# Kernel tuning notes

Hardware: AMD Instinct MI355X
Metric: run time of the kernel (lower is better)

The kernel has to match this reference:

```python
import jax, jax.numpy as jnp
import numpy as np

N = 50000      # num nodes
E = 1_600_000  # num edges
D = 64         # in_dim == hidden_dim
H = 4          # heads
C = 16         # head_dim = hidden_dim // heads
NEG = 0.2      # leaky_relu negative slope (PyG GATConv default)


def setup_inputs() -> dict:
    key = jax.random.key(0)
    ks = jax.random.split(key, 20)
    f = lambda k, s: (jax.random.normal(k, s, jnp.float32) * 0.1)
    return dict(
        node_features=jax.random.normal(ks[0], (N, D), jnp.float32),
        edge_index=jax.random.randint(ks[1], (2, E), 0, N, dtype=jnp.int32),
        edge_type=jax.random.randint(ks[2], (E,), 0, 5, dtype=jnp.int32),
        edge_attr=jax.random.normal(ks[3], (E, 1), jnp.float32),
        # GAT layer 1 (PyG GATConv: lin has no bias, att_* are [H,C], final bias [H*C])
        W1=f(ks[4], (D, H * C)), att_src1=f(ks[5], (H, C)), att_dst1=f(ks[6], (H, C)),
        We1=f(ks[7], (1, H * C)), att_e1=f(ks[8], (H, C)), b1=jnp.zeros((H * C,), jnp.float32),
        # GAT layer 2
        W2=f(ks[9], (D, H * C)), att_src2=f(ks[10], (H, C)), att_dst2=f(ks[11], (H, C)),
        We2=f(ks[12], (1, H * C)), att_e2=f(ks[13], (H, C)), b2=jnp.zeros((H * C,), jnp.float32),
        # LayerNorms
        g1=jnp.ones((D,), jnp.float32), beta1=jnp.zeros((D,), jnp.float32),
        g2=jnp.ones((D,), jnp.float32), beta2=jnp.zeros((D,), jnp.float32),
        # output head
        Wout=f(ks[14], (D, 1)), bout=jnp.zeros((1,), jnp.float32),
    )


def _layernorm(x, g, b, eps=1e-5):
    mu = x.mean(-1, keepdims=True)
    v = ((x - mu) ** 2).mean(-1, keepdims=True)
    return (x - mu) * jax.lax.rsqrt(v + eps) * g + b


def _seg_softmax(alpha, dst, n):
    # numerically stable segment softmax over incoming edges of each dst node
    m = jax.ops.segment_max(alpha, dst, num_segments=n)
    m = jnp.where(jnp.isfinite(m), m, 0.0)
    ex = jnp.exp(alpha - m[dst])
    den = jax.ops.segment_sum(ex, dst, num_segments=n)
    return ex / (den[dst] + 1e-16)


def _gatconv(x, src, dst, eattr, W, a_s, a_d, We, a_e, b, n):
    xs = (x @ W).reshape(n, H, C)                       # [N,H,C]
    a_src = jnp.einsum('nhc,hc->nh', xs, a_s)           # [N,H]
    a_dst = jnp.einsum('nhc,hc->nh', xs, a_d)           # [N,H]
    ee = (eattr @ We).reshape(-1, H, C)                 # [E',H,C]
    a_edge = jnp.einsum('ehc,hc->eh', ee, a_e)          # [E',H]
    alpha = a_src[src] + a_dst[dst] + a_edge            # [E',H]
    alpha = jax.nn.leaky_relu(alpha, NEG)
    alpha = _seg_softmax(alpha, dst, n)                 # [E',H]
    msg = xs[src] * alpha[..., None]                    # [E',H,C] gather-weighted messages
    out = jax.ops.segment_sum(msg, dst, num_segments=n) # scatter-aggregate
    return out.reshape(n, H * C) + b


def reference(node_features, edge_index, edge_type, edge_attr,
              W1, att_src1, att_dst1, We1, att_e1, b1,
              W2, att_src2, att_dst2, We2, att_e2, b2,
              g1, beta1, g2, beta2, Wout, bout):
    src, dst = edge_index[0], edge_index[1]
    # PyG add_self_loops(fill_value='mean'): self-loop edge_attr = mean of edge_attr over incoming edges
    cnt = jax.ops.segment_sum(jnp.ones((E,), jnp.float32), dst, num_segments=N)
    loop_attr = jax.ops.segment_sum(edge_attr, dst, num_segments=N) / jnp.maximum(cnt, 1.0)[:, None]
    loops = jnp.arange(N, dtype=src.dtype)
    src2 = jnp.concatenate([src, loops])
    dst2 = jnp.concatenate([dst, loops])
    ea = jnp.concatenate([edge_attr, loop_attr], axis=0)

    residual = node_features  # in_dim == hidden_dim -> no res_proj
    h = _gatconv(node_features, src2, dst2, ea, W1, att_src1, att_dst1, We1, att_e1, b1, N)
    h = jax.nn.elu(_layernorm(h + residual, g1, beta1))
    residual = h
    h = _gatconv(h, src2, dst2, ea, W2, att_src2, att_dst2, We2, att_e2, b2, N)
    h = jax.nn.elu(_layernorm(h + residual, g2, beta2))
    return h @ Wout + bout
```

## Files before the change

### kernel.cpp

```cpp
#include <hip/hip_runtime.h>
#include <hip/hip_bf16.h>
#include <cfloat>

#define NN 50000
#define NE 1600000
#define NEG 0.2f
#define NBKT 1563
#define BNODE 32
#define P1_TILE 2048
#define P1_BLOCKS 782
#define BCAP 1280
#define SLOTS 96
#define L2E 1.4426950408889634f

typedef __attribute__((ext_vector_type(8))) short bf8_t;
typedef __attribute__((ext_vector_type(4))) float f4_t;

__device__ __forceinline__ float bf16bits_to_f(unsigned v) {
  return __uint_as_float(v << 16);
}
__device__ __forceinline__ unsigned f_to_bf16bits(float f) {
  unsigned u = __float_as_uint(f);
  return (u + 0x7fffu + ((u >> 16) & 1u)) >> 16;
}

__global__ __launch_bounds__(256) void prep_kernel(
    const float* __restrict__ W1, const float* __restrict__ as1,
    const float* __restrict__ ad1, unsigned short* __restrict__ We1,
    const float* __restrict__ W2, const float* __restrict__ as2,
    const float* __restrict__ ad2, unsigned short* __restrict__ We2) {
  const float* W = blockIdx.x ? W2 : W1;
  const float* as = blockIdx.x ? as2 : as1;
  const float* ad = blockIdx.x ? ad2 : ad1;
  unsigned short* Wx = blockIdx.x ? We2 : We1;
  int t = threadIdx.x;
  if (t < 64) {
    const float* wr = W + t * 64;
#pragma unroll
    for (int h = 0; h < 4; ++h) {
      float ps = 0.f, pd = 0.f;
#pragma unroll
      for (int c = 0; c < 16; ++c) {
        ps = fmaf(wr[h * 16 + c], as[h * 16 + c], ps);
        pd = fmaf(wr[h * 16 + c], ad[h * 16 + c], pd);
      }
      Wx[t * 80 + 64 + h] = (unsigned short)f_to_bf16bits(ps * L2E);
      Wx[t * 80 + 68 + h] = (unsigned short)f_to_bf16bits(pd * L2E);
    }
#pragma unroll
    for (int j = 72; j < 80; ++j) Wx[t * 80 + j] = 0;
  }
  for (int i = t; i < 4096; i += 256) {
    int k = i >> 6, n = i & 63;
    Wx[k * 80 + n] = (unsigned short)f_to_bf16bits(W[i]);
  }
}

__global__ __launch_bounds__(256) void bin_kernel(
    const int* __restrict__ src, const int* __restrict__ dst,
    const float* __restrict__ ea, int* __restrict__ gcnt,
    int2* __restrict__ gbuf) {
  __shared__ int lcnt[NBKT];
  __shared__ int lcur[NBKT];
  int t = threadIdx.x;
  for (int i = t; i < NBKT; i += 256) lcnt[i] = 0;
  __syncthreads();
  int e0 = blockIdx.x * P1_TILE;
  int bb[8], vx[8], vy[8];
#pragma unroll
  for (int k = 0; k < 8; ++k) {
    int e = e0 + k * 256 + t;
    if (e < NE) {
      int d = dst[e];
      bb[k] = d >> 5;
      vx[k] = ((d & 31) << 16) | src[e];
      vy[k] = __float_as_int(ea[e]);
      atomicAdd(&lcnt[bb[k]], 1);
    } else {
      bb[k] = -1;
    }
  }
  __syncthreads();
  for (int i = t; i < NBKT; i += 256) lcur[i] = atomicAdd(&gcnt[i], lcnt[i]);
  __syncthreads();
#pragma unroll
  for (int k = 0; k < 8; ++k) {
    if (bb[k] >= 0) {
      int pos = atomicAdd(&lcur[bb[k]], 1);
      if (pos < BCAP) gbuf[(size_t)bb[k] * BCAP + pos] = make_int2(vx[k], vy[k]);
    }
  }
}

__global__ __launch_bounds__(256) void build_kernel(
    const int* __restrict__ gcnt, const int2* __restrict__ gbuf,
    int* __restrict__ cnt, unsigned* __restrict__ csr) {
  __shared__ int lc[BNODE];
  int t = threadIdx.x;
  int b = blockIdx.x;
  if (t < BNODE) lc[t] = 0;
  __syncthreads();
  int len = gcnt[b]; if (len > BCAP) len = BCAP;
  const int2* buf = gbuf + (size_t)b * BCAP;
  for (int i = t; i < len; i += 256) {
    int2 v = buf[i];
    int dl = (v.x >> 16) & 31;
    int s = v.x & 0xffff;
    int pos = atomicAdd(&lc[dl], 1);
    if (pos < SLOTS) {
      unsigned eb = ((unsigned)v.y) & 0xffff0000u;
      csr[(size_t)(b * BNODE + dl) * SLOTS + pos] = eb | (unsigned)s;
    }
  }
  __syncthreads();
  if (t < BNODE) {
    int n = b * BNODE + t;
    if (n < NN) cnt[n] = min(lc[t], SLOTS);
  }
}

__device__ __forceinline__ bf8_t pack8(const float* p) {
  bf8_t r;
#pragma unroll
  for (int i = 0; i < 8; ++i) r[i] = (short)f_to_bf16bits(p[i]);
  return r;
}

template <bool FP32IN>
__global__ __launch_bounds__(256) void gemm_mfma_kernel(
    const void* __restrict__ xin, const unsigned short* __restrict__ Wext,
    unsigned short* __restrict__ xsb, float* __restrict__ a_src,
    float* __restrict__ a_dst) {
  __shared__ unsigned short Wt[80][68];
  int t = threadIdx.x;
  for (int i = t; i < 5120; i += 256) {
    int k = i / 80, n = i - k * 80;
    Wt[n][k] = Wext[i];
  }
  __syncthreads();
  int lane = t & 63, wave = t >> 6;
  int quad = lane >> 4, n16 = lane & 15;

  bf8_t bfrag[5][2];
#pragma unroll
  for (int nt = 0; nt < 5; ++nt)
#pragma unroll
    for (int kk = 0; kk < 2; ++kk)
      bfrag[nt][kk] = *(const bf8_t*)&Wt[nt * 16 + n16][kk * 32 + quad * 8];

  int r0 = blockIdx.x * 64 + wave * 16;
  int rowA = r0 + n16; if (rowA > NN - 1) rowA = NN - 1;
  bf8_t af0, af1;
  if (FP32IN) {
    const float* xr = (const float*)xin + (size_t)rowA * 64 + quad * 8;
    af0 = pack8(xr);
    af1 = pack8(xr + 32);
  } else {
    const bf8_t* xrow =
        (const bf8_t*)((const unsigned short*)xin + (size_t)rowA * 64);
    af0 = xrow[quad];
    af1 = xrow[4 + quad];
  }
#pragma unroll
  for (int nt = 0; nt < 5; ++nt) {
    f4_t acc = {0.f, 0.f, 0.f, 0.f};
    acc = __builtin_amdgcn_mfma_f32_16x16x32_bf16(af0, bfrag[nt][0], acc, 0, 0, 0);
    acc = __builtin_amdgcn_mfma_f32_16x16x32_bf16(af1, bfrag[nt][1], acc, 0, 0, 0);
    if (nt < 4) {
#pragma unroll
      for (int reg = 0; reg < 4; ++reg) {
        int row = r0 + quad * 4 + reg;
        if (row < NN)
          xsb[(size_t)row * 64 + nt * 16 + n16] =
              (unsigned short)f_to_bf16bits(acc[reg]);
      }
    } else {
#pragma unroll
      for (int reg = 0; reg < 4; ++reg) {
        int row = r0 + quad * 4 + reg;
        if (row < NN && n16 < 8) {
          if (n16 < 4) a_src[row * 4 + n16] = acc[reg];
          else a_dst[row * 4 + (n16 - 4)] = acc[reg];
        }
      }
    }
  }
}

template <bool HEAD>
__global__ __launch_bounds__(256) void aggregate_kernel(
    const int* __restrict__ cnt, const unsigned* __restrict__ csr,
    const unsigned short* __restrict__ xsb, const float* __restrict__ a_src,
    const float* __restrict__ a_dst, const float* __restrict__ We,
    const float* __restrict__ att_e, const float* __restrict__ bias,
    const float* __restrict__ res, const float* __restrict__ g,
    const float* __restrict__ beta, const float* __restrict__ Wout,
    const float* __restrict__ bout, float* __restrict__ out,
    unsigned short* __restrict__ out_b) {
  __shared__ __align__(16) uint2 rec[4][64][4];
  int t = threadIdx.x;
  int lane = t & 63, wave = t >> 6;
  int n = blockIdx.x * 4 + wave;
  int d2 = lane & 31;
  int hb = d2 >> 3;
  int half = lane >> 5;

  float sp = We[lane] * att_e[lane];
#pragma unroll
  for (int off = 8; off; off >>= 1) sp += __shfl_xor(sp, off, 16);
  sp *= L2E;
  float s0 = __shfl(sp, 0, 64), s1 = __shfl(sp, 16, 64);
  float s2 = __shfl(sp, 32, 64), s3 = __shfl(sp, 48, 64);

  const float4 adv = *(const float4*)(a_dst + (size_t)n * 4);

  int dn = cnt[n];
  int r0 = n * SLOTS, r1 = r0 + dn;
  float accx = 0.f, accy = 0.f, den = 0.f, easum = 0.f;
  const uint2* rpb = &rec[wave][half][hb];
  const char* xd = (const char*)xsb + d2 * 4;

  for (int base = r0; base < r1; base += 64) {
    int c = r1 - base; if (c > 64) c = 64;
    int e = base + lane;
    unsigned ce = (e < r1) ? csr[e] : 0u;
    float ea = __uint_as_float(ce & 0xffff0000u);
    easum += ea;
    unsigned soff = (ce & 0xffffu) * 128u;
    float ex0 = 0.f, ex1 = 0.f, ex2 = 0.f, ex3 = 0.f;
    if (e < r1) {
      const float4 av = *(const float4*)(a_src + (size_t)(ce & 0xffffu) * 4);
      float a0 = av.x + fmaf(ea, s0, adv.x); a0 = fmaxf(a0, NEG * a0);
      float a1 = av.y + fmaf(ea, s1, adv.y); a1 = fmaxf(a1, NEG * a1);
      float a2 = av.z + fmaf(ea, s2, adv.z); a2 = fmaxf(a2, NEG * a2);
      float a3 = av.w + fmaf(ea, s3, adv.w); a3 = fmaxf(a3, NEG * a3);
      ex0 = exp2f(a0); ex1 = exp2f(a1); ex2 = exp2f(a2); ex3 = exp2f(a3);
    }
    uint4* wp = (uint4*)&rec[wave][lane][0];
    wp[0] = make_uint4(soff, __float_as_uint(ex0), soff, __float_as_uint(ex1));
    wp[1] = make_uint4(soff, __float_as_uint(ex2), soff, __float_as_uint(ex3));
    int c8 = (c + 7) & ~7;
    for (int j = 0; j < c8; j += 8) {
      uint2 va = rpb[j * 4];
      uint2 vb = rpb[j * 4 + 8];
      uint2 vc = rpb[j * 4 + 16];
      uint2 vd = rpb[j * 4 + 24];
      unsigned ua = *(const unsigned*)(xd + va.x);
      unsigned ub = *(const unsigned*)(xd + vb.x);
      unsigned uc = *(const unsigned*)(xd + vc.x);
      unsigned ud = *(const unsigned*)(xd + vd.x);
      float efa = __uint_as_float(va.y), efb = __uint_as_float(vb.y);
      float efc = __uint_as_float(vc.y), efd = __uint_as_float(vd.y);
      den += (efa + efb) + (efc + efd);
      accx = fmaf(efa, __uint_as_float(ua << 16), accx);
      accy = fmaf(efa, __uint_as_float(ua & 0xffff0000u), accy);
      accx = fmaf(efb, __uint_as_float(ub << 16), accx);
      accy = fmaf(efb, __uint_as_float(ub & 0xffff0000u), accy);
      accx = fmaf(efc, __uint_as_float(uc << 16), accx);
      accy = fmaf(efc, __uint_as_float(uc & 0xffff0000u), accy);
      accx = fmaf(efd, __uint_as_float(ud << 16), accx);
      accy = fmaf(efd, __uint_as_float(ud & 0xffff0000u), accy);
    }
  }

  den += __shfl_xor(den, 32, 64);
  accx += __shfl_xor(accx, 32, 64);
  accy += __shfl_xor(accy, 32, 64);
#pragma unroll
  for (int off = 32; off; off >>= 1) easum += __shfl_xor(easum, off, 64);

  float loop_ea = easum / fmaxf((float)dn, 1.0f);
  float as_h = a_src[(size_t)n * 4 + hb];
  float adn = (hb == 0) ? adv.x : (hb == 1) ? adv.y : (hb == 2) ? adv.z : adv.w;
  float sph = (hb == 0) ? s0 : (hb == 1) ? s1 : (hb == 2) ? s2 : s3;
  float a_self = as_h + fmaf(loop_ea, sph, adn);
  a_self = fmaxf(a_self, NEG * a_self);
  float ex_self = exp2f(a_self);
  den += ex_self;
  unsigned un = *(const unsigned*)((const char*)xsb + (size_t)n * 128 + d2 * 4);
  accx = fmaf(ex_self, __uint_as_float(un << 16), accx);
  accy = fmaf(ex_self, __uint_as_float(un & 0xffff0000u), accy);

  float rden = 1.f / (den + 1e-16f);
  const float2 bi = *(const float2*)(bias + d2 * 2);
  const float2 rsd = *(const float2*)(res + (size_t)n * 64 + d2 * 2);
  float vx = accx * rden + bi.x + rsd.x;
  float vy = accy * rden + bi.y + rsd.y;
  float s = vx + vy;
#pragma unroll
  for (int off = 32; off; off >>= 1) s += __shfl_xor(s, off, 64);
  float mu = s * (1.0f / 128.0f);
  float dx = vx - mu, dy = vy - mu;
  float var = dx * dx + dy * dy;
#pragma unroll
  for (int off = 32; off; off >>= 1) var += __shfl_xor(var, off, 64);
  var *= (1.0f / 128.0f);
  float rstd = rsqrtf(var + 1e-5f);
  const float2 gg = *(const float2*)(g + d2 * 2);
  const float2 bb = *(const float2*)(beta + d2 * 2);
  float yx = dx * rstd * gg.x + bb.x;
  float yy = dy * rstd * gg.y + bb.y;
  yx = yx > 0.f ? yx : expm1f(yx);
  yy = yy > 0.f ? yy : expm1f(yy);
  if (HEAD) {
    const float2 wv = *(const float2*)(Wout + d2 * 2);
    float p = yx * wv.x + yy * wv.y;
#pragma unroll
    for (int off = 32; off; off >>= 1) p += __shfl_xor(p, off, 64);
    if (lane == 0) out[n] = p * 0.5f + bout[0];
  } else if (lane < 32) {
    *(float2*)(out + (size_t)n * 64 + d2 * 2) = make_float2(yx, yy);
    unsigned ob = f_to_bf16bits(yx) | (f_to_bf16bits(yy) << 16);
    *(unsigned*)(out_b + (size_t)n * 64 + d2 * 2) = ob;
  }
}

extern "C" void kernel_launch(void* const* d_in, const int* in_sizes, int n_in,
                              void* d_out, int out_size, void* d_ws,
                              size_t ws_size, hipStream_t stream) {
  const float* node_features = (const float*)d_in[0];
  const int* edge_index = (const int*)d_in[1];
  const int* src = edge_index;
  const int* dst = edge_index + NE;
  const float* edge_attr = (const float*)d_in[3];
  const float* W1 = (const float*)d_in[4];
  const float* att_src1 = (const float*)d_in[5];
  const float* att_dst1 = (const float*)d_in[6];
  const float* We1 = (const float*)d_in[7];
  const float* att_e1 = (const float*)d_in[8];
  const float* b1 = (const float*)d_in[9];
  const float* W2 = (const float*)d_in[10];
  const float* att_src2 = (const float*)d_in[11];
  const float* att_dst2 = (const float*)d_in[12];
  const float* We2 = (const float*)d_in[13];
  const float* att_e2 = (const float*)d_in[14];
  const float* b2 = (const float*)d_in[15];
  const float* g1 = (const float*)d_in[16];
  const float* beta1 = (const float*)d_in[17];
  const float* g2 = (const float*)d_in[18];
  const float* beta2 = (const float*)d_in[19];
  const float* Wout = (const float*)d_in[20];
  const float* bout = (const float*)d_in[21];
  float* out = (float*)d_out;

  char* ws = (char*)d_ws;
  size_t o = 0;
  auto alloc = [&](size_t bytes) {
    void* p = ws + o;
    o += (bytes + 255) & ~(size_t)255;
    return p;
  };
  int* gcnt = (int*)alloc((size_t)NBKT * 4);
  int2* gbuf = (int2*)alloc((size_t)NBKT * BCAP * 8);
  int* cnt = (int*)alloc((size_t)NN * 4);
  unsigned* csr = (unsigned*)alloc((size_t)NN * SLOTS * 4);
  unsigned short* xsb = (unsigned short*)alloc((size_t)NN * 64 * 2);
  unsigned short* h1b = (unsigned short*)alloc((size_t)NN * 64 * 2);
  unsigned short* Wext1 = (unsigned short*)alloc(64 * 80 * 2);
  unsigned short* Wext2 = (unsigned short*)alloc(64 * 80 * 2);
  float* a_srcb = (float*)alloc((size_t)NN * 4 * 4);
  float* a_dstb = (float*)alloc((size_t)NN * 4 * 4);
  float* h1 = (float*)alloc((size_t)NN * 64 * 4);

  hipMemsetAsync(gcnt, 0, (size_t)NBKT * 4, stream);

  prep_kernel<<<2, 256, 0, stream>>>(W1, att_src1, att_dst1, Wext1, W2,
                                     att_src2, att_dst2, Wext2);

  bin_kernel<<<P1_BLOCKS, 256, 0, stream>>>(src, dst, edge_attr, gcnt, gbuf);
  build_kernel<<<NBKT, 256, 0, stream>>>(gcnt, gbuf, cnt, csr);

  gemm_mfma_kernel<true><<<782, 256, 0, stream>>>(node_features, Wext1, xsb,
                                                  a_srcb, a_dstb);
  aggregate_kernel<false><<<NN / 4, 256, 0, stream>>>(
      cnt, csr, xsb, a_srcb, a_dstb, We1, att_e1, b1, node_features, g1, beta1,
      nullptr, nullptr, h1, h1b);

  gemm_mfma_kernel<false><<<782, 256, 0, stream>>>(h1b, Wext2, xsb, a_srcb,
                                                   a_dstb);
  aggregate_kernel<true><<<NN / 4, 256, 0, stream>>>(
      cnt, csr, xsb, a_srcb, a_dstb, We2, att_e2, b2, h1, g2, beta2, Wout, bout,
      out, nullptr);
}
```

Measured before the change: 266.6 us.

## Fuse prep into GEMM, merge binning with first GEMM, drop fp32 h1

Removes the separate weight-prep kernel: each GEMM block now converts W to bf16 and computes the attention projection columns in shared memory. The edge-binning and first-layer GEMM run as one horizontally fused launch with disjoint block ranges. The layer-1 output is no longer written in fp32, and layer 2 reads its residual from the bf16 copy. This saves two launches and one large write/read, but each GEMM block repeats the weight preprocessing, and the residual loses precision by being stored in bf16.

New measurement: 255.4 us. 4.2% less time.

```diff
diff --git a/kernel.cpp b/kernel.cpp
--- a/kernel.cpp
+++ b/kernel.cpp
@@ -9,9 +9,11 @@
 #define BNODE 32
 #define P1_TILE 2048
 #define P1_BLOCKS 782
+#define GEMM_BLOCKS 782
 #define BCAP 1280
 #define SLOTS 96
 #define L2E 1.4426950408889634f
+#define SMEM_BYTES 12512
 
 typedef __attribute__((ext_vector_type(8))) short bf8_t;
 typedef __attribute__((ext_vector_type(4))) float f4_t;
@@ -24,48 +26,23 @@
   return (u + 0x7fffu + ((u >> 16) & 1u)) >> 16;
 }
 
-__global__ __launch_bounds__(256) void prep_kernel(
-    const float* __restrict__ W1, const float* __restrict__ as1,
-    const float* __restrict__ ad1, unsigned short* __restrict__ We1,
-    const float* __restrict__ W2, const float* __restrict__ as2,
-    const float* __restrict__ ad2, unsigned short* __restrict__ We2) {
-  const float* W = blockIdx.x ? W2 : W1;
-  const float* as = blockIdx.x ? as2 : as1;
-  const float* ad = blockIdx.x ? ad2 : ad1;
-  unsigned short* Wx = blockIdx.x ? We2 : We1;
-  int t = threadIdx.x;
-  if (t < 64) {
-    const float* wr = W + t * 64;
-#pragma unroll
-    for (int h = 0; h < 4; ++h) {
-      float ps = 0.f, pd = 0.f;
-#pragma unroll
-      for (int c = 0; c < 16; ++c) {
-        ps = fmaf(wr[h * 16 + c], as[h * 16 + c], ps);
-        pd = fmaf(wr[h * 16 + c], ad[h * 16 + c], pd);
-      }
-      Wx[t * 80 + 64 + h] = (unsigned short)f_to_bf16bits(ps * L2E);
-      Wx[t * 80 + 68 + h] = (unsigned short)f_to_bf16bits(pd * L2E);
-    }
-#pragma unroll
-    for (int j = 72; j < 80; ++j) Wx[t * 80 + j] = 0;
-  }
-  for (int i = t; i < 4096; i += 256) {
-    int k = i >> 6, n = i & 63;
-    Wx[k * 80 + n] = (unsigned short)f_to_bf16bits(W[i]);
-  }
-}
-
-__global__ __launch_bounds__(256) void bin_kernel(
-    const int* __restrict__ src, const int* __restrict__ dst,
-    const float* __restrict__ ea, int* __restrict__ gcnt,
-    int2* __restrict__ gbuf) {
-  __shared__ int lcnt[NBKT];
-  __shared__ int lcur[NBKT];
+__device__ __forceinline__ bf8_t pack8(const float* p) {
+  bf8_t r;
+#pragma unroll
+  for (int i = 0; i < 8; ++i) r[i] = (short)f_to_bf16bits(p[i]);
+  return r;
+}
+
+__device__ void bin_body(char* smem, int blk, const int* __restrict__ src,
+                         const int* __restrict__ dst,
+                         const float* __restrict__ ea, int* __restrict__ gcnt,
+                         int2* __restrict__ gbuf) {
+  int* lcnt = (int*)smem;
+  int* lcur = lcnt + NBKT;
   int t = threadIdx.x;
   for (int i = t; i < NBKT; i += 256) lcnt[i] = 0;
   __syncthreads();
-  int e0 = blockIdx.x * P1_TILE;
+  int e0 = blk * P1_TILE;
   int bb[8], vx[8], vy[8];
 #pragma unroll
   for (int k = 0; k < 8; ++k) {
@@ -92,50 +69,34 @@
   }
 }
 
-__global__ __launch_bounds__(256) void build_kernel(
-    const int* __restrict__ gcnt, const int2* __restrict__ gbuf,
-    int* __restrict__ cnt, unsigned* __restrict__ csr) {
-  __shared__ int lc[BNODE];
+template <bool FP32IN>
+__device__ void gemm_body(char* smem, int blk, const void* __restrict__ xin,
+                          const float* __restrict__ W,
+                          const float* __restrict__ att_s,
+                          const float* __restrict__ att_d,
+                          unsigned short* __restrict__ xsb,
+                          float* __restrict__ a_src,
+                          float* __restrict__ a_dst) {
+  unsigned short(*Wt)[68] = (unsigned short(*)[68])smem;
   int t = threadIdx.x;
-  int b = blockIdx.x;
-  if (t < BNODE) lc[t] = 0;
-  __syncthreads();
-  int len = gcnt[b]; if (len > BCAP) len = BCAP;
-  const int2* buf = gbuf + (size_t)b * BCAP;
-  for (int i = t; i < len; i += 256) {
-    int2 v = buf[i];
-    int dl = (v.x >> 16) & 31;
-    int s = v.x & 0xffff;
-    int pos = atomicAdd(&lc[dl], 1);
-    if (pos < SLOTS) {
-      unsigned eb = ((unsigned)v.y) & 0xffff0000u;
-      csr[(size_t)(b * BNODE + dl) * SLOTS + pos] = eb | (unsigned)s;
-    }
-  }
-  __syncthreads();
-  if (t < BNODE) {
-    int n = b * BNODE + t;
-    if (n < NN) cnt[n] = min(lc[t], SLOTS);
-  }
-}
-
-__device__ __forceinline__ bf8_t pack8(const float* p) {
-  bf8_t r;
-#pragma unroll
-  for (int i = 0; i < 8; ++i) r[i] = (short)f_to_bf16bits(p[i]);
-  return r;
-}
-
-template <bool FP32IN>
-__global__ __launch_bounds__(256) void gemm_mfma_kernel(
-    const void* __restrict__ xin, const unsigned short* __restrict__ Wext,
-    unsigned short* __restrict__ xsb, float* __restrict__ a_src,
-    float* __restrict__ a_dst) {
-  __shared__ unsigned short Wt[80][68];
-  int t = threadIdx.x;
-  for (int i = t; i < 5120; i += 256) {
-    int k = i / 80, n = i - k * 80;
-    Wt[n][k] = Wext[i];
+  for (int i = t; i < 4096; i += 256) {
+    int k = i >> 6, n = i & 63;
+    Wt[n][k] = (unsigned short)f_to_bf16bits(W[i]);
+  }
+  __syncthreads();
+  {
+    int k = t & 63, h = t >> 6;
+    float ps = 0.f, pd = 0.f;
+#pragma unroll
+    for (int c = 0; c < 16; ++c) {
+      float w = bf16bits_to_f(Wt[h * 16 + c][k]);
+      ps = fmaf(w, att_s[h * 16 + c], ps);
+      pd = fmaf(w, att_d[h * 16 + c], pd);
+    }
+    Wt[64 + h][k] = (unsigned short)f_to_bf16bits(ps * L2E);
+    Wt[68 + h][k] = (unsigned short)f_to_bf16bits(pd * L2E);
+    Wt[72 + h][k] = 0;
+    Wt[76 + h][k] = 0;
   }
   __syncthreads();
   int lane = t & 63, wave = t >> 6;
@@ -148,7 +109,7 @@
     for (int kk = 0; kk < 2; ++kk)
       bfrag[nt][kk] = *(const bf8_t*)&Wt[nt * 16 + n16][kk * 32 + quad * 8];
 
-  int r0 = blockIdx.x * 64 + wave * 16;
+  int r0 = blk * 64 + wave * 16;
   int rowA = r0 + n16; if (rowA > NN - 1) rowA = NN - 1;
   bf8_t af0, af1;
   if (FP32IN) {
@@ -187,13 +148,65 @@
   }
 }
 
+__global__ __launch_bounds__(256) void front_kernel(
+    const int* __restrict__ src, const int* __restrict__ dst,
+    const float* __restrict__ ea, int* __restrict__ gcnt,
+    int2* __restrict__ gbuf, const float* __restrict__ x,
+    const float* __restrict__ W1, const float* __restrict__ as1,
+    const float* __restrict__ ad1, unsigned short* __restrict__ xsb,
+    float* __restrict__ a_src, float* __restrict__ a_dst) {
+  __shared__ __align__(16) char smem[SMEM_BYTES];
+  if (blockIdx.x < P1_BLOCKS) {
+    bin_body(smem, blockIdx.x, src, dst, ea, gcnt, gbuf);
+  } else {
+    gemm_body<true>(smem, blockIdx.x - P1_BLOCKS, x, W1, as1, ad1, xsb, a_src,
+                    a_dst);
+  }
+}
+
+__global__ __launch_bounds__(256) void gemm2_kernel(
+    const unsigned short* __restrict__ xin, const float* __restrict__ W,
+    const float* __restrict__ att_s, const float* __restrict__ att_d,
+    unsigned short* __restrict__ xsb, float* __restrict__ a_src,
+    float* __restrict__ a_dst) {
+  __shared__ __align__(16) char smem[SMEM_BYTES];
+  gemm_body<false>(smem, blockIdx.x, xin, W, att_s, att_d, xsb, a_src, a_dst);
+}
+
+__global__ __launch_bounds__(256) void build_kernel(
+    const int* __restrict__ gcnt, const int2* __restrict__ gbuf,
+    int* __restrict__ cnt, unsigned* __restrict__ csr) {
+  __shared__ int lc[BNODE];
+  int t = threadIdx.x;
+  int b = blockIdx.x;
+  if (t < BNODE) lc[t] = 0;
+  __syncthreads();
+  int len = gcnt[b]; if (len > BCAP) len = BCAP;
+  const int2* buf = gbuf + (size_t)b * BCAP;
+  for (int i = t; i < len; i += 256) {
+    int2 v = buf[i];
+    int dl = (v.x >> 16) & 31;
+    int s = v.x & 0xffff;
+    int pos = atomicAdd(&lc[dl], 1);
+    if (pos < SLOTS) {
+      unsigned eb = ((unsigned)v.y) & 0xffff0000u;
+      csr[(size_t)(b * BNODE + dl) * SLOTS + pos] = eb | (unsigned)s;
+    }
+  }
+  __syncthreads();
+  if (t < BNODE) {
+    int n = b * BNODE + t;
+    if (n < NN) cnt[n] = min(lc[t], SLOTS);
+  }
+}
+
 template <bool HEAD>
 __global__ __launch_bounds__(256) void aggregate_kernel(
     const int* __restrict__ cnt, const unsigned* __restrict__ csr,
     const unsigned short* __restrict__ xsb, const float* __restrict__ a_src,
     const float* __restrict__ a_dst, const float* __restrict__ We,
     const float* __restrict__ att_e, const float* __restrict__ bias,
-    const float* __restrict__ res, const float* __restrict__ g,
+    const void* __restrict__ resv, const float* __restrict__ g,
     const float* __restrict__ beta, const float* __restrict__ Wout,
     const float* __restrict__ bout, float* __restrict__ out,
     unsigned short* __restrict__ out_b) {
@@ -283,7 +296,15 @@
 
   float rden = 1.f / (den + 1e-16f);
   const float2 bi = *(const float2*)(bias + d2 * 2);
-  const float2 rsd = *(const float2*)(res + (size_t)n * 64 + d2 * 2);
+  float2 rsd;
+  if (HEAD) {
+    unsigned ur =
+        *(const unsigned*)((const unsigned short*)resv + (size_t)n * 64 + d2 * 2);
+    rsd.x = bf16bits_to_f(ur & 0xffffu);
+    rsd.y = __uint_as_float(ur & 0xffff0000u);
+  } else {
+    rsd = *(const float2*)((const float*)resv + (size_t)n * 64 + d2 * 2);
+  }
   float vx = accx * rden + bi.x + rsd.x;
   float vy = accy * rden + bi.y + rsd.y;
   float s = vx + vy;
@@ -309,7 +330,6 @@
     for (int off = 32; off; off >>= 1) p += __shfl_xor(p, off, 64);
     if (lane == 0) out[n] = p * 0.5f + bout[0];
   } else if (lane < 32) {
-    *(float2*)(out + (size_t)n * 64 + d2 * 2) = make_float2(yx, yy);
     unsigned ob = f_to_bf16bits(yx) | (f_to_bf16bits(yy) << 16);
     *(unsigned*)(out_b + (size_t)n * 64 + d2 * 2) = ob;
   }
@@ -356,29 +376,23 @@
   unsigned* csr = (unsigned*)alloc((size_t)NN * SLOTS * 4);
   unsigned short* xsb = (unsigned short*)alloc((size_t)NN * 64 * 2);
   unsigned short* h1b = (unsigned short*)alloc((size_t)NN * 64 * 2);
-  unsigned short* Wext1 = (unsigned short*)alloc(64 * 80 * 2);
-  unsigned short* Wext2 = (unsigned short*)alloc(64 * 80 * 2);
   float* a_srcb = (float*)alloc((size_t)NN * 4 * 4);
   float* a_dstb = (float*)alloc((size_t)NN * 4 * 4);
-  float* h1 = (float*)alloc((size_t)NN * 64 * 4);
 
   hipMemsetAsync(gcnt, 0, (size_t)NBKT * 4, stream);
 
-  prep_kernel<<<2, 256, 0, stream>>>(W1, att_src1, att_dst1, Wext1, W2,
-                                     att_src2, att_dst2, Wext2);
-
-  bin_kernel<<<P1_BLOCKS, 256, 0, stream>>>(src, dst, edge_attr, gcnt, gbuf);
+  front_kernel<<<P1_BLOCKS + GEMM_BLOCKS, 256, 0, stream>>>(
+      src, dst, edge_attr, gcnt, gbuf, node_features, W1, att_src1, att_dst1,
+      xsb, a_srcb, a_dstb);
   build_kernel<<<NBKT, 256, 0, stream>>>(gcnt, gbuf, cnt, csr);
 
-  gemm_mfma_kernel<true><<<782, 256, 0, stream>>>(node_features, Wext1, xsb,
-                                                  a_srcb, a_dstb);
   aggregate_kernel<false><<<NN / 4, 256, 0, stream>>>(
       cnt, csr, xsb, a_srcb, a_dstb, We1, att_e1, b1, node_features, g1, beta1,
-      nullptr, nullptr, h1, h1b);
-
-  gemm_mfma_kernel<false><<<782, 256, 0, stream>>>(h1b, Wext2, xsb, a_srcb,
-                                                   a_dstb);
+      nullptr, nullptr, nullptr, h1b);
+
+  gemm2_kernel<<<GEMM_BLOCKS, 256, 0, stream>>>(h1b, W2, att_src2, att_dst2,
+                                                xsb, a_srcb, a_dstb);
   aggregate_kernel<true><<<NN / 4, 256, 0, stream>>>(
-      cnt, csr, xsb, a_srcb, a_dstb, We2, att_e2, b2, h1, g2, beta2, Wout, bout,
-      out, nullptr);
-}
+      cnt, csr, xsb, a_srcb, a_dstb, We2, att_e2, b2, h1b, g2, beta2, Wout,
+      bout, out, nullptr);
+}
```
